# Kernel tuning notes

Hardware: AMD Instinct MI355X
Metric: run time of the kernel (lower is better)

The kernel has to match this reference:

```python
import jax, jax.numpy as jnp
import numpy as np

N_MICS = 8
MIC_RADIUS = 0.05
SAMPLE_RATE = 16000.0
SPEED_SOUND = 343.0
EPS = 1e-20
SPHERE_LEVELS = 4


def sphere_np(levels=SPHERE_LEVELS):
    # Faithful numpy port of the torch icosphere subdivision in sphere().
    h = 5.0 ** 0.5 / 5.0
    r = 2.0 / 5.0 * 5.0 ** 0.5
    pi = 3.141592654
    pts = np.zeros((12, 3), dtype=np.float32)
    pts[0] = [0.0, 0.0, 1.0]
    pts[11] = [0.0, 0.0, -1.0]
    k = np.arange(5, dtype=np.float32)
    pts[1:6, 0] = r * np.sin(2.0 * pi * k / 5.0)
    pts[1:6, 1] = r * np.cos(2.0 * pi * k / 5.0)
    pts[1:6, 2] = h
    pts[6:11, 0] = -r * np.sin(2.0 * pi * k / 5.0)
    pts[6:11, 1] = -r * np.cos(2.0 * pi * k / 5.0)
    pts[6:11, 2] = -h
    trs = np.array([[0, 2, 1], [0, 3, 2], [0, 4, 3], [0, 5, 4], [0, 1, 5],
                    [9, 1, 2], [10, 2, 3], [6, 3, 4], [7, 4, 5], [8, 5, 1],
                    [4, 7, 6], [5, 8, 7], [1, 9, 8], [2, 10, 9], [3, 6, 10],
                    [11, 6, 7], [11, 7, 8], [11, 8, 9], [11, 9, 10], [11, 10, 6]], dtype=np.int64)
    for _ in range(levels):
        T = trs.shape[0]
        sub = np.zeros((4 * T, 6), dtype=np.int64)
        sub[0 * T:1 * T] = trs[:, [0, 0, 0, 1, 2, 0]]
        sub[1 * T:2 * T] = trs[:, [0, 1, 1, 1, 1, 2]]
        sub[2 * T:3 * T] = trs[:, [2, 0, 1, 2, 2, 2]]
        sub[3 * T:4 * T] = trs[:, [0, 1, 1, 2, 2, 0]]
        flat = np.concatenate((sub[:, [0, 1]], sub[:, [2, 3]], sub[:, [4, 5]]), axis=0)
        srt = np.sort(flat, axis=1)
        m = srt.max()
        scal = srt[:, 0] * (m + 1) + srt[:, 1]
        uniq, inv = np.unique(scal, return_inverse=True)
        uv0 = uniq // (m + 1)
        uv1 = uniq - uv0 * (m + 1)
        trs = inv.reshape(3, -1).T
        pts = pts[uv0] + pts[uv1]
        pts /= np.sqrt((pts ** 2).sum(axis=1, keepdims=True))
    return pts.astype(np.float32)


def setup_inputs() -> dict:
    key = jax.random.key(0)
    # DOA grid and TDOAs from array geometry (precomputed in SrpPhat.__init__)
    doas_np = sphere_np()                                    # [2562, 3]
    ang = 2.0 * np.pi * np.arange(N_MICS) / N_MICS
    mics_np = np.stack([MIC_RADIUS * np.cos(ang), MIC_RADIUS * np.sin(ang),
                        np.zeros(N_MICS)], axis=1).astype(np.float32)  # [8, 3]
    taus_np = (SAMPLE_RATE / SPEED_SOUND) * (doas_np @ mics_np.T)      # [2562, 8]
    B, T, F, P = 4, 250, 513, N_MICS * (N_MICS + 1) // 2
    XXs = jax.random.normal(key, (B, T, F, 2, P), dtype=jnp.float32)
    return {"XXs": XXs, "taus": jnp.asarray(taus_np), "doas": jnp.asarray(doas_np)}


def reference(XXs, taus, doas):
    B, T, F, _, P = XXs.shape
    n_mics = taus.shape[1]
    D = taus.shape[0]
    frame_size = (F - 1) * 2
    # Steering phases: a = exp(-j * omega * tau)   [D, F, M]
    omegas = 2.0 * jnp.pi * jnp.arange(F, dtype=jnp.float32) / frame_size
    phase = omegas[None, :, None] * taus[:, None, :]
    A_re = jnp.cos(phase)
    A_im = -jnp.sin(phase)
    # Cross steering terms for every mic pair (triu incl. diagonal): W = a_i * conj(a_j)^H form
    i0, i1 = np.triu_indices(n_mics)                         # 36 pairs for 8 mics
    Ws_re = A_re[:, :, i0] * A_re[:, :, i1] + A_im[:, :, i0] * A_im[:, :, i1]  # [D, F, P]
    Ws_im = A_re[:, :, i0] * A_im[:, :, i1] - A_im[:, :, i0] * A_re[:, :, i1]
    # PHAT normalization of the cross-spectra
    XX_re = XXs[:, :, :, 0, :]
    XX_im = XXs[:, :, :, 1, :]
    mag = jnp.sqrt(XX_re ** 2 + XX_im ** 2) + EPS
    Xr = (XX_re / mag).reshape(B, T, F * P)
    Xi = (XX_im / mag).reshape(B, T, F * P)
    Wr = Ws_re.reshape(D, F * P)
    Wi = Ws_im.reshape(D, F * P)
    # SRP map: Re{ sum_fp XX_norm * conj(W) } reduced over freqs and pairs
    Ys = jnp.matmul(Xr, Wr.T) + jnp.matmul(Xi, Wi.T)         # [B, T, D]
    idx = jnp.argmax(Ys, axis=2)                             # [B, T]
    return doas[idx]                                         # [B, T, 3]
```

## Files before the change

kernel.cpp:

```cpp
#include <hip/hip_runtime.h>
#include <math.h>


#define F_BINS  513
#define M_TOTAL 1000
#define D_TOTAL 2562
#define D_PAD   2688
#define NPAIR   28
#define NC      32
#define K2      (NPAIR * NC)
#define S_SCALE 4.67f
#define NBT     4
#define CNT     4
#define FSPLIT  12
#define KSPB    4
#define KPS     224
#define BT_PAD  1024
#define DBLK    11

#define OFF_COEF 0
#define OFF_TT   16512
#define OFF_GT   (OFF_TT + (size_t)K2 * D_PAD)
#define OFF_GP   (OFF_GT + (size_t)K2 * BT_PAD)
#define OFF_YS   OFF_GP

__device__ __constant__ int c_ptab[NPAIR] = {1,2,3,4,5,6,7, 9,10,11,12,13,14,
                                             16,17,18,19,20, 22,23,24,25,
                                             27,28,29, 31,32, 34};
__device__ __constant__ int c_i0[NPAIR] = {0,0,0,0,0,0,0, 1,1,1,1,1,1,
                                           2,2,2,2,2, 3,3,3,3, 4,4,4, 5,5, 6};
__device__ __constant__ int c_i1[NPAIR] = {1,2,3,4,5,6,7, 2,3,4,5,6,7,
                                           3,4,5,6,7, 4,5,6,7, 5,6,7, 6,7, 7};

__global__ void k_init(const float* __restrict__ taus,
                       float* __restrict__ coefEO, float* __restrict__ Tt) {
    __shared__ double sHC[NC][NC + 1];
    __shared__ double sHS[NC][NC + 1];
    if (blockIdx.x < DBLK * NPAIR) {
        const int p = blockIdx.x / DBLK;
        const int d = (blockIdx.x % DBLK) * 256 + threadIdx.x;
        if (d >= D_PAD) return;
        const bool live = d < D_TOTAL;
        const int dd = live ? d : 0;
        const float u = (taus[dd * 8 + c_i0[p]] - taus[dd * 8 + c_i1[p]]) * (1.0f / S_SCALE);
        float* base = Tt + (size_t)p * 32 * D_PAD + d;
        base[0] = live ? 1.f : 0.f;
        base[(size_t)16 * D_PAD] = live ? u : 0.f;
        float tp = 1.f, tc = u;
        const float u2 = 2.f * u;
        for (int n = 2; n < NC; ++n) {
            float tn = u2 * tc - tp;
            tp = tc; tc = tn;
            int c = (n & 1) ? 16 + (n >> 1) : (n >> 1);
            base[(size_t)c * D_PAD] = live ? tn : 0.f;
        }
    } else {
        const int f = blockIdx.x - DBLK * NPAIR;
        const int t = threadIdx.x;
        if (t < 32) {
            const double z = (double)f * (M_PI / 512.0) * (double)S_SCALE;
            double th = M_PI * (t + 0.5) / NC;
            double ct = cos(th);
            double hs, hc;
            sincos(z * ct, &hs, &hc);
            double cp = 1.0, cc = ct, c2 = 2.0 * ct;
            sHC[0][t] = hc;      sHS[0][t] = hs;
            sHC[1][t] = hc * cc; sHS[1][t] = hs * cc;
            for (int n = 2; n < NC; ++n) {
                double cn = c2 * cc - cp;
                cp = cc; cc = cn;
                sHC[n][t] = hc * cn;
                sHS[n][t] = hs * cn;
            }
        }
        __syncthreads();
        if (t < 32) {
            const int n = (t < 16) ? 2 * t : 2 * (t - 16) + 1;
            double sum = 0.0;
            if (t < 16) { for (int j = 0; j < NC; ++j) sum += sHC[n][j]; }
            else        { for (int j = 0; j < NC; ++j) sum += sHS[n][j]; }
            double scale = (n == 0) ? (1.0 / NC) : (2.0 / NC);
            coefEO[f * 32 + t] = (float)(sum * scale);
        }
    }
}

#define NSLOTA 3
__global__ __launch_bounds__(128, 3) void k_stageA(
    const float* __restrict__ XXs, const float* __restrict__ coefEO,
    float* __restrict__ Gp)
{
    __shared__ float sRaw[2][NBT * CNT * 72];
    __shared__ float sCall[44][32];
    const int t     = threadIdx.x;
    const int bt0   = blockIdx.x * NBT;
    const int split = blockIdx.y;
    const int fbeg  = (F_BINS * split) / FSPLIT;
    const int fend  = (F_BINS * (split + 1)) / FSPLIT;
    const int nf     = fend - fbeg;
    const int nchunk = (nf + CNT - 1) / CNT;
    const int p   = t & 31;
    const int sel = t >> 5;
    const bool im = sel >= 2;
    const int c0  = (sel & 1) * 8 + (im ? 16 : 0);
    const int qq  = c_ptab[p < NPAIR ? p : NPAIR - 1];

    for (int e = t; e < 44 * 8; e += 128) {
        int fl = e >> 3, q = e & 7;
        float4 v = {0.f, 0.f, 0.f, 0.f};
        if (fl < nf) v = *(const float4*)&coefEO[(fbeg + fl) * 32 + q * 4];
        *(float4*)&sCall[fl][q * 4] = v;
    }

    const float* srcp[NSLOTA];
    int fls[NSLOTA];
    #pragma unroll
    for (int s = 0; s < NSLOTA; ++s) {
        int e  = t + s * 128;
        int ec = e < 288 ? e : 0;
        int bta = ec / 72, ra = ec - bta * 72;
        fls[s]  = ra / 18;
        srcp[s] = XXs + ((size_t)(bt0 + bta) * F_BINS) * 72 + ra * 4;
    }

    float acc[NBT][8] = {};

    auto stage = [&](int fc, int b) {
        #pragma unroll
        for (int s = 0; s < NSLOTA; ++s) {
            if (t + s * 128 < 288) {
                const int fcs = min(fc, 512 - fls[s]);
                __builtin_amdgcn_global_load_lds(
                    (const __attribute__((address_space(1))) void*)(srcp[s] + (size_t)fcs * 72),
                    (__attribute__((address_space(3))) void*)(&sRaw[b][(t + s * 128) * 4]),
                    16, 0, 0);
            }
        }
    };
    auto compute = [&](int fc, int b) {
        const int cbase = fc - fbeg;
        const float* rb = &sRaw[b][0];
        float4 cjA[4], cjB[4];
        #pragma unroll
        for (int j = 0; j < 4; ++j) {
            cjA[j] = *(const float4*)&sCall[cbase + j][c0];
            cjB[j] = *(const float4*)&sCall[cbase + j][c0 + 4];
        }
        #pragma unroll
        for (int bt = 0; bt < NBT; ++bt) {
            #pragma unroll
            for (int j = 0; j < 4; ++j) {
                const float* ep = rb + bt * 288 + j * 72 + qq;
                float xr = ep[0], xi = ep[36];
                float inv = rsqrtf(xr * xr + xi * xi + 1e-37f);
                float a = (im ? xi : xr) * inv;
                acc[bt][0] = fmaf(a, cjA[j].x, acc[bt][0]);
                acc[bt][1] = fmaf(a, cjA[j].y, acc[bt][1]);
                acc[bt][2] = fmaf(a, cjA[j].z, acc[bt][2]);
                acc[bt][3] = fmaf(a, cjA[j].w, acc[bt][3]);
                acc[bt][4] = fmaf(a, cjB[j].x, acc[bt][4]);
                acc[bt][5] = fmaf(a, cjB[j].y, acc[bt][5]);
                acc[bt][6] = fmaf(a, cjB[j].z, acc[bt][6]);
                acc[bt][7] = fmaf(a, cjB[j].w, acc[bt][7]);
            }
        }
    };

    stage(fbeg, 0);
    __syncthreads();
    for (int i = 0; i < nchunk; ++i) {
        const int b  = i & 1;
        const int fc = fbeg + i * CNT;
        if (i + 1 < nchunk) stage(fc + CNT, b ^ 1);
        compute(fc, b);
        __syncthreads();
    }

    if (p < NPAIR) {
        float* gsp = Gp + (size_t)split * M_TOTAL * K2;
        #pragma unroll
        for (int bt = 0; bt < NBT; ++bt) {
            float* g = gsp + (size_t)(bt0 + bt) * K2 + p * 32 + c0;
            float4 v0 = {acc[bt][0], acc[bt][1], acc[bt][2], acc[bt][3]};
            float4 v1 = {acc[bt][4], acc[bt][5], acc[bt][6], acc[bt][7]};
            *(float4*)&g[0] = v0;
            *(float4*)&g[4] = v1;
        }
    }
}

__global__ __launch_bounds__(256) void k_reduceG(
    const float* __restrict__ Gp, float* __restrict__ Gt)
{
    __shared__ float sT[32][65];
    const int t   = threadIdx.x;
    const int k0  = blockIdx.x * 32;
    const int bt0 = blockIdx.y * 64;
    const size_t MK = (size_t)M_TOTAL * K2;
    #pragma unroll
    for (int i = 0; i < 8; ++i) {
        int e  = t + i * 256;
        int kl = e & 31, btl = e >> 5;
        int bt = bt0 + btl;
        float s = 0.f;
        if (bt < M_TOTAL) {
            const float* g = Gp + (size_t)bt * K2 + k0 + kl;
            #pragma unroll
            for (int pl = 0; pl < FSPLIT; ++pl) s += g[pl * MK];
        }
        sT[kl][btl] = s;
    }
    __syncthreads();
    #pragma unroll
    for (int i = 0; i < 8; ++i) {
        int e   = t + i * 256;
        int btl = e & 63, kl = e >> 6;
        Gt[(size_t)(k0 + kl) * BT_PAD + bt0 + btl] = sT[kl][btl];
    }
}

#define BKB 32
__global__ __launch_bounds__(256, 4) void k_gemmB(
    const float* __restrict__ Gt, const float* __restrict__ Tt,
    float* __restrict__ Ysp)
{
    __shared__ float sA[BKB][260];
    __shared__ float sB[BKB][68];
    const int t = threadIdx.x;
    const int row0 = blockIdx.x * 256;
    const int col0 = blockIdx.y * 64;
    const int koff = blockIdx.z * KPS;
    const int tx = t & 15;
    const int ty = t >> 4;
    float acc[16][4] = {};

    for (int k0 = 0; k0 < KPS; k0 += BKB) {
        __syncthreads();
        #pragma unroll
        for (int i = 0; i < 8; ++i) {
            int e = t + i * 256;
            int kk = e >> 6, r4 = (e & 63) * 4;
            *(float4*)&sA[kk][r4] =
                *(const float4*)&Gt[(size_t)(koff + k0 + kk) * BT_PAD + row0 + r4];
        }
        #pragma unroll
        for (int i = 0; i < 2; ++i) {
            int e = t + i * 256;
            int kk = e >> 4, c4 = (e & 15) * 4;
            *(float4*)&sB[kk][c4] =
                *(const float4*)&Tt[(size_t)(koff + k0 + kk) * D_PAD + col0 + c4];
        }
        __syncthreads();
        #pragma unroll 8
        for (int kk = 0; kk < BKB; ++kk) {
            float4 b  = *(const float4*)&sB[kk][tx * 4];
            float4 a0 = *(const float4*)&sA[kk][ty * 16];
            float4 a1 = *(const float4*)&sA[kk][ty * 16 + 4];
            float4 a2 = *(const float4*)&sA[kk][ty * 16 + 8];
            float4 a3 = *(const float4*)&sA[kk][ty * 16 + 12];
            float av[16] = {a0.x, a0.y, a0.z, a0.w, a1.x, a1.y, a1.z, a1.w,
                            a2.x, a2.y, a2.z, a2.w, a3.x, a3.y, a3.z, a3.w};
            float bv[4] = {b.x, b.y, b.z, b.w};
            #pragma unroll
            for (int i = 0; i < 16; ++i)
                #pragma unroll
                for (int j = 0; j < 4; ++j)
                    acc[i][j] = fmaf(av[i], bv[j], acc[i][j]);
        }
    }
    float* yp = Ysp + (size_t)blockIdx.z * M_TOTAL * D_PAD;
    #pragma unroll
    for (int i = 0; i < 16; ++i) {
        int rg = row0 + ty * 16 + i;
        if (rg >= M_TOTAL) continue;
        float4 v = {acc[i][0], acc[i][1], acc[i][2], acc[i][3]};
        *(float4*)(yp + (size_t)rg * D_PAD + col0 + tx * 4) = v;
    }
}

__global__ __launch_bounds__(256) void k_argmax(
    const float* __restrict__ Ysp, const float* __restrict__ doas,
    float* __restrict__ out)
{
    __shared__ float sv[256];
    __shared__ int   si[256];
    const int row = blockIdx.x;
    const int tid = threadIdx.x;
    const float* y = Ysp + (size_t)row * D_PAD;
    const size_t PL = (size_t)M_TOTAL * D_PAD;
    float best = -INFINITY;
    int bi = D_TOTAL;
    for (int d = tid; d < D_TOTAL; d += 256) {
        float v = y[d] + y[d + PL] + y[d + 2 * PL] + y[d + 3 * PL];
        if (v > best) { best = v; bi = d; }
    }
    sv[tid] = best; si[tid] = bi;
    __syncthreads();
    for (int s = 128; s > 0; s >>= 1) {
        if (tid < s) {
            float v2 = sv[tid + s]; int i2 = si[tid + s];
            if (v2 > sv[tid] || (v2 == sv[tid] && i2 < si[tid])) { sv[tid] = v2; si[tid] = i2; }
        }
        __syncthreads();
    }
    if (tid == 0) {
        int idx = si[0];
        out[row * 3 + 0] = doas[idx * 3 + 0];
        out[row * 3 + 1] = doas[idx * 3 + 1];
        out[row * 3 + 2] = doas[idx * 3 + 2];
    }
}

extern "C" void kernel_launch(void* const* d_in, const int* in_sizes, int n_in,
                              void* d_out, int out_size, void* d_ws, size_t ws_size,
                              hipStream_t stream) {
    const float* XXs  = (const float*)d_in[0];
    const float* taus = (const float*)d_in[1];
    const float* doas = (const float*)d_in[2];
    float* ws     = (float*)d_ws;
    float* coefEO = ws + OFF_COEF;
    float* Tt     = ws + OFF_TT;
    float* Gt     = ws + OFF_GT;
    float* Gp     = ws + OFF_GP;
    float* Ysp    = ws + OFF_YS;

    k_init   <<<DBLK * NPAIR + F_BINS, 256, 0, stream>>>(taus, coefEO, Tt);
    k_stageA <<<dim3(M_TOTAL / NBT, FSPLIT), 128, 0, stream>>>(XXs, coefEO, Gp);
    k_reduceG<<<dim3(K2 / 32, BT_PAD / 64), 256, 0, stream>>>(Gp, Gt);
    k_gemmB  <<<dim3(BT_PAD / 256, D_PAD / 64, KSPB), 256, 0, stream>>>(Gt, Tt, Ysp);
    k_argmax <<<M_TOTAL, 256, 0, stream>>>(Ysp, doas, (float*)d_out);
}
```

Baseline: 322.6 us.

## Make stage-A waves independent with per-wave buffers and no block barrier

Each 64-lane wave in k_stageA now owns four batch-time rows and its own double-buffered LDS staging area. That lets the per-chunk __syncthreads be replaced by a wave-local vmcnt wait and a sched barrier. Each thread now accumulates both the real and imaginary coefficient halves (16 accumulators), and the frequency chunk shrinks from 4 to 2. This aims to remove block-wide barrier stalls and let waves run out of step, at the cost of more registers per thread and half as many blocks in the grid.

```diff
diff --git a/kernel.cpp b/kernel.cpp
--- a/kernel.cpp
+++ b/kernel.cpp
@@ -11,12 +11,14 @@
 #define K2      (NPAIR * NC)
 #define S_SCALE 4.67f
 #define NBT     4
-#define CNT     4
+#define CNT     2
+#define WPB     2
 #define FSPLIT  12
 #define KSPB    4
 #define KPS     224
 #define BT_PAD  1024
 #define DBLK    11
+#define SLOTS   (NBT * CNT * 18)
 
 #define OFF_COEF 0
 #define OFF_TT   16512
@@ -85,25 +87,24 @@
     }
 }
 
-#define NSLOTA 3
 __global__ __launch_bounds__(128, 3) void k_stageA(
     const float* __restrict__ XXs, const float* __restrict__ coefEO,
     float* __restrict__ Gp)
 {
-    __shared__ float sRaw[2][NBT * CNT * 72];
+    __shared__ float sRaw[WPB][2][NBT * CNT * 72];
     __shared__ float sCall[44][32];
     const int t     = threadIdx.x;
-    const int bt0   = blockIdx.x * NBT;
+    const int wave  = t >> 6;
+    const int lane  = t & 63;
     const int split = blockIdx.y;
     const int fbeg  = (F_BINS * split) / FSPLIT;
     const int fend  = (F_BINS * (split + 1)) / FSPLIT;
     const int nf     = fend - fbeg;
     const int nchunk = (nf + CNT - 1) / CNT;
-    const int p   = t & 31;
-    const int sel = t >> 5;
-    const bool im = sel >= 2;
-    const int c0  = (sel & 1) * 8 + (im ? 16 : 0);
-    const int qq  = c_ptab[p < NPAIR ? p : NPAIR - 1];
+    const int btg0  = (blockIdx.x * WPB + wave) * NBT;
+    const int p     = lane & 31;
+    const int half  = lane >> 5;
+    const int qq    = c_ptab[p < NPAIR ? p : NPAIR - 1];
 
     for (int e = t; e < 44 * 8; e += 128) {
         int fl = e >> 3, q = e & 7;
@@ -112,56 +113,64 @@
         *(float4*)&sCall[fl][q * 4] = v;
     }
 
-    const float* srcp[NSLOTA];
-    int fls[NSLOTA];
+    const float* srcp[3];
+    int fls[3];
     #pragma unroll
-    for (int s = 0; s < NSLOTA; ++s) {
-        int e  = t + s * 128;
-        int ec = e < 288 ? e : 0;
-        int bta = ec / 72, ra = ec - bta * 72;
-        fls[s]  = ra / 18;
-        srcp[s] = XXs + ((size_t)(bt0 + bta) * F_BINS) * 72 + ra * 4;
-    }
-
-    float acc[NBT][8] = {};
+    for (int s = 0; s < 3; ++s) {
+        int e  = lane + s * 64;
+        int ec = e < SLOTS ? e : 0;
+        int bta = ec / 36, rem = ec - bta * 36;
+        fls[s]  = rem / 18;
+        srcp[s] = XXs + ((size_t)(btg0 + bta) * F_BINS) * 72 + rem * 4;
+    }
+
+    float acc[NBT][16] = {};
 
     auto stage = [&](int fc, int b) {
-        #pragma unroll
-        for (int s = 0; s < NSLOTA; ++s) {
-            if (t + s * 128 < 288) {
+        float* dst = &sRaw[wave][b][0];
+        #pragma unroll
+        for (int s = 0; s < 3; ++s) {
+            if (s < 2 || lane < 16) {
                 const int fcs = min(fc, 512 - fls[s]);
                 __builtin_amdgcn_global_load_lds(
                     (const __attribute__((address_space(1))) void*)(srcp[s] + (size_t)fcs * 72),
-                    (__attribute__((address_space(3))) void*)(&sRaw[b][(t + s * 128) * 4]),
+                    (__attribute__((address_space(3))) void*)(dst + (lane + s * 64) * 4),
                     16, 0, 0);
             }
         }
     };
+
     auto compute = [&](int fc, int b) {
-        const int cbase = fc - fbeg;
-        const float* rb = &sRaw[b][0];
-        float4 cjA[4], cjB[4];
-        #pragma unroll
-        for (int j = 0; j < 4; ++j) {
-            cjA[j] = *(const float4*)&sCall[cbase + j][c0];
-            cjB[j] = *(const float4*)&sCall[cbase + j][c0 + 4];
-        }
-        #pragma unroll
-        for (int bt = 0; bt < NBT; ++bt) {
+        const float* rb = &sRaw[wave][b][0];
+        #pragma unroll
+        for (int fl = 0; fl < CNT; ++fl) {
+            const int cr = fc - fbeg + fl;
+            float4 cA0 = *(const float4*)&sCall[cr][half * 8];
+            float4 cA1 = *(const float4*)&sCall[cr][half * 8 + 4];
+            float4 cB0 = *(const float4*)&sCall[cr][16 + half * 8];
+            float4 cB1 = *(const float4*)&sCall[cr][16 + half * 8 + 4];
             #pragma unroll
-            for (int j = 0; j < 4; ++j) {
-                const float* ep = rb + bt * 288 + j * 72 + qq;
+            for (int bt = 0; bt < NBT; ++bt) {
+                const float* ep = rb + bt * (CNT * 72) + fl * 72 + qq;
                 float xr = ep[0], xi = ep[36];
                 float inv = rsqrtf(xr * xr + xi * xi + 1e-37f);
-                float a = (im ? xi : xr) * inv;
-                acc[bt][0] = fmaf(a, cjA[j].x, acc[bt][0]);
-                acc[bt][1] = fmaf(a, cjA[j].y, acc[bt][1]);
-                acc[bt][2] = fmaf(a, cjA[j].z, acc[bt][2]);
-                acc[bt][3] = fmaf(a, cjA[j].w, acc[bt][3]);
-                acc[bt][4] = fmaf(a, cjB[j].x, acc[bt][4]);
-                acc[bt][5] = fmaf(a, cjB[j].y, acc[bt][5]);
-                acc[bt][6] = fmaf(a, cjB[j].z, acc[bt][6]);
-                acc[bt][7] = fmaf(a, cjB[j].w, acc[bt][7]);
+                float ar = xr * inv, ai = xi * inv;
+                acc[bt][0]  = fmaf(ar, cA0.x, acc[bt][0]);
+                acc[bt][1]  = fmaf(ar, cA0.y, acc[bt][1]);
+                acc[bt][2]  = fmaf(ar, cA0.z, acc[bt][2]);
+                acc[bt][3]  = fmaf(ar, cA0.w, acc[bt][3]);
+                acc[bt][4]  = fmaf(ar, cA1.x, acc[bt][4]);
+                acc[bt][5]  = fmaf(ar, cA1.y, acc[bt][5]);
+                acc[bt][6]  = fmaf(ar, cA1.z, acc[bt][6]);
+                acc[bt][7]  = fmaf(ar, cA1.w, acc[bt][7]);
+                acc[bt][8]  = fmaf(ai, cB0.x, acc[bt][8]);
+                acc[bt][9]  = fmaf(ai, cB0.y, acc[bt][9]);
+                acc[bt][10] = fmaf(ai, cB0.z, acc[bt][10]);
+                acc[bt][11] = fmaf(ai, cB0.w, acc[bt][11]);
+                acc[bt][12] = fmaf(ai, cB1.x, acc[bt][12]);
+                acc[bt][13] = fmaf(ai, cB1.y, acc[bt][13]);
+                acc[bt][14] = fmaf(ai, cB1.z, acc[bt][14]);
+                acc[bt][15] = fmaf(ai, cB1.w, acc[bt][15]);
             }
         }
     };
@@ -173,18 +182,23 @@
         const int fc = fbeg + i * CNT;
         if (i + 1 < nchunk) stage(fc + CNT, b ^ 1);
         compute(fc, b);
-        __syncthreads();
+        asm volatile("s_waitcnt vmcnt(0)" ::: "memory");
+        __builtin_amdgcn_sched_barrier(0);
     }
 
     if (p < NPAIR) {
         float* gsp = Gp + (size_t)split * M_TOTAL * K2;
         #pragma unroll
         for (int bt = 0; bt < NBT; ++bt) {
-            float* g = gsp + (size_t)(bt0 + bt) * K2 + p * 32 + c0;
-            float4 v0 = {acc[bt][0], acc[bt][1], acc[bt][2], acc[bt][3]};
-            float4 v1 = {acc[bt][4], acc[bt][5], acc[bt][6], acc[bt][7]};
-            *(float4*)&g[0] = v0;
-            *(float4*)&g[4] = v1;
+            float* g = gsp + (size_t)(btg0 + bt) * K2 + p * 32 + half * 8;
+            float4 v0 = {acc[bt][0],  acc[bt][1],  acc[bt][2],  acc[bt][3]};
+            float4 v1 = {acc[bt][4],  acc[bt][5],  acc[bt][6],  acc[bt][7]};
+            float4 v2 = {acc[bt][8],  acc[bt][9],  acc[bt][10], acc[bt][11]};
+            float4 v3 = {acc[bt][12], acc[bt][13], acc[bt][14], acc[bt][15]};
+            *(float4*)&g[0]  = v0;
+            *(float4*)&g[4]  = v1;
+            *(float4*)&g[16] = v2;
+            *(float4*)&g[20] = v3;
         }
     }
 }
@@ -325,7 +339,7 @@
     float* Ysp    = ws + OFF_YS;
 
     k_init   <<<DBLK * NPAIR + F_BINS, 256, 0, stream>>>(taus, coefEO, Tt);
-    k_stageA <<<dim3(M_TOTAL / NBT, FSPLIT), 128, 0, stream>>>(XXs, coefEO, Gp);
+    k_stageA <<<dim3(M_TOTAL / (NBT * WPB), FSPLIT), 128, 0, stream>>>(XXs, coefEO, Gp);
     k_reduceG<<<dim3(K2 / 32, BT_PAD / 64), 256, 0, stream>>>(Gp, Gt);
     k_gemmB  <<<dim3(BT_PAD / 256, D_PAD / 64, KSPB), 256, 0, stream>>>(Gt, Tt, Ysp);
     k_argmax <<<M_TOTAL, 256, 0, stream>>>(Ysp, doas, (float*)d_out);
```

New measurement: 317.4 us. No clear change (-1.6%).
